# Performance work log

Hardware: AMD Instinct MI355X
Metric: run time of the kernel (lower is better)

Reference implementation:

```python
import jax, jax.numpy as jnp
import numpy as np

# ---- static config (from init_kwargs) ----
XB = (-51.2, 51.2, 0.8); YB = (-51.2, 51.2, 0.8); ZB = (-10.0, 10.0, 20.0); DB = (1.0, 60.0, 1.0)
OGH, OGW = 256, 704          # image_size
DS = 16                      # downsample
C_IN, C_TR = 512, 64         # numC_input, numC_trans
B, N = 2, 6                  # batch, cameras
FH, FW = (OGH + DS - 1) // DS, (OGW + DS - 1) // DS   # 16, 44
DBINS = int(np.arange(DB[0], DB[1], DB[2]).shape[0])  # 59 depth bins
NX = int(round((XB[1] - XB[0]) / XB[2]))              # 128
NY = int(round((YB[1] - YB[0]) / YB[2]))              # 128
NZ = int(round((ZB[1] - ZB[0]) / ZB[2]))              # 1
START = jnp.array([XB[0], YB[0], ZB[0]], jnp.float32)
INTERVAL = jnp.array([XB[2], YB[2], ZB[2]], jnp.float32)

def make_frustum():
    ds = np.arange(DB[0], DB[1], DB[2], dtype=np.float32)            # [D]
    xs = np.linspace(0.0, OGW - 1, FW, dtype=np.float32)             # [FW]
    ys = np.linspace(0.0, OGH - 1, FH, dtype=np.float32)             # [FH]
    x, y, d = np.broadcast_arrays(xs[None, None, :], ys[None, :, None], ds[:, None, None])
    return jnp.asarray(np.stack([x, y, d], -1))                      # [D,FH,FW,3]

FRUSTUM = make_frustum()


def setup_inputs() -> dict:
    key = jax.random.key(0)
    k1, k2, k3 = jax.random.split(key, 3)
    x = jax.random.normal(k1, (B, N, C_IN, FH, FW), jnp.float32)
    # camera->ego rotation: cam z -> ego x, cam x -> -ego y, cam y -> -ego z
    R = jnp.array([[0., 0., 1.], [-1., 0., 0.], [0., -1., 0.]], jnp.float32)
    rots = jnp.broadcast_to(R, (B, N, 3, 3))
    trans = 0.5 * jax.random.normal(k2, (B, N, 3), jnp.float32)
    K = jnp.array([[500., 0., OGW / 2.], [0., 500., OGH / 2.], [0., 0., 1.]], jnp.float32)
    intrins = jnp.broadcast_to(K, (B, N, 3, 3))
    fan = C_IN + DBINS + C_TR
    w_depth = jax.random.normal(k3, (DBINS + C_TR, C_IN), jnp.float32) * np.float32(np.sqrt(2.0 / fan))
    b_depth = jnp.zeros((DBINS + C_TR,), jnp.float32)
    return {"x": x, "rots": rots, "trans": trans, "intrins": intrins,
            "w_depth": w_depth, "b_depth": b_depth}


def reference(x, rots, trans, intrins, w_depth, b_depth):
    # ---- geometry: frustum pixel coords -> ego frame (get_geometry) ----
    pts = jnp.concatenate([FRUSTUM[..., :2] * FRUSTUM[..., 2:3], FRUSTUM[..., 2:3]], -1)  # [D,FH,FW,3]
    combine = rots @ jnp.linalg.inv(intrins)                                              # [B,N,3,3]
    geom = jnp.einsum('bnij,dhwj->bndhwi', combine, pts) + trans[:, :, None, None, None, :]
    # ---- depth-weighted feature volume (get_volume) ----
    xf = x.reshape(B * N, C_IN, FH, FW)
    feat = jnp.einsum('oc,bchw->bohw', w_depth, xf) + b_depth[None, :, None, None]        # 1x1 conv
    depth = jax.nn.softmax(feat[:, :DBINS], axis=1)                                       # [BN,D,H,W]
    ctx = feat[:, DBINS:DBINS + C_TR]                                                     # [BN,C,H,W]
    vol = depth[:, None] * ctx[:, :, None]                                                # [BN,C,D,H,W]
    vol = vol.reshape(B, N, C_TR, DBINS, FH, FW).transpose(0, 1, 3, 4, 5, 2)              # [B,N,D,H,W,C]
    # ---- voxel pooling: sort/cumsum trick == per-voxel segment-sum scatter ----
    g = jnp.trunc((geom - START) / INTERVAL).astype(jnp.int32).reshape(-1, 3)             # trunc == torch .long()
    P = g.shape[0]
    b_ix = jnp.repeat(jnp.arange(B, dtype=jnp.int32), P // B)
    kept = ((g[:, 0] >= 0) & (g[:, 0] < NX) & (g[:, 1] >= 0) & (g[:, 1] < NY)
            & (g[:, 2] >= 0) & (g[:, 2] < NZ))
    total = B * NZ * NX * NY
    flat = ((b_ix * NZ + g[:, 2]) * NX + g[:, 0]) * NY + g[:, 1]                          # bev[b,gz,gx,gy]
    flat = jnp.where(kept, flat, total)                                                   # invalid -> dummy slot
    feats = jnp.where(kept[:, None], vol.reshape(-1, C_TR), 0.0)
    bev = jnp.zeros((total + 1, C_TR), vol.dtype).at[flat].add(feats)[:total]
    bev = bev.reshape(B, NZ, NX, NY, C_TR).transpose(0, 4, 1, 2, 3)                       # [B,C,NZ,NX,NY]
    return bev.reshape(B, C_TR * NZ, NX, NY)
```

## Files before the change

### kernel.cpp

```cpp
#include <hip/hip_runtime.h>
#include <cstddef>
#include <cstdint>
#include <math.h>

#define C_IN   512
#define C_TR   64
#define DBINS  59
#define NO     123
#define NOP    128
#define FH     16
#define FW     44
#define NPIX   704
#define NCAM   6
#define NBATCH 2
#define NBN    12
#define NXG    128
#define NYG    128
#define NCH    4
#define KCH    (C_IN/NCH)

#define WS_CMB     0
#define WS_XS      128
#define WS_YS      176

#define WSP_WT     256
#define WT_SZ      (C_IN*NOP)
#define WSP_PART   (WSP_WT + WT_SZ)
#define PART_SZ    (NCH*NBN*NPIX*NOP)
#define WSP_DEP    (WSP_PART + PART_SZ)
#define DEP_SZ     (NBN*NPIX*C_TR)
#define WSP_CTX    (WSP_DEP + DEP_SZ)
#define WSP_BEV    (WSP_CTX + DEP_SZ)
#define BEV_SZ     (NBATCH*NXG*NYG*C_TR)
#define WS_FAST_TOTALF (WSP_BEV + BEV_SZ)

#define WS_FEAT    256
#define WS_CTX     (WS_FEAT + NBN*NOP*NPIX)
#define WS_BEV     (WS_CTX + NBN*NPIX*C_TR)

__device__ void prep_body(const float* __restrict__ rots,
                          const float* __restrict__ intrins,
                          float* __restrict__ wsf, int t)
{
#pragma clang fp contract(off)
  if (t < NBN) {
    const float* K = intrins + t * 9;
    const float* R = rots + t * 9;
    float A[3][3] = {{K[0],K[1],K[2]},{K[3],K[4],K[5]},{K[6],K[7],K[8]}};
    int piv[3] = {0,1,2};
    for (int k = 0; k < 2; ++k) {
      int p = k; float mx = fabsf(A[k][k]);
      for (int r = k+1; r < 3; ++r) { float v = fabsf(A[r][k]); if (v > mx) { mx = v; p = r; } }
      if (p != k) {
        for (int j = 0; j < 3; ++j) { float tmp = A[k][j]; A[k][j] = A[p][j]; A[p][j] = tmp; }
        int ti = piv[k]; piv[k] = piv[p]; piv[p] = ti;
      }
      float rk = 1.0f / A[k][k];
      for (int r = k+1; r < 3; ++r) {
        float l = A[r][k] * rk;
        A[r][k] = l;
        for (int j = k+1; j < 3; ++j) A[r][j] = A[r][j] - l * A[k][j];
      }
    }
    float r0 = 1.0f / A[0][0], r1 = 1.0f / A[1][1], r2 = 1.0f / A[2][2];
    float inv[3][3];
    for (int j = 0; j < 3; ++j) {
      float b0 = (piv[0]==j) ? 1.0f : 0.0f;
      float b1 = (piv[1]==j) ? 1.0f : 0.0f;
      float b2 = (piv[2]==j) ? 1.0f : 0.0f;
      float y0 = b0;
      float y1 = b1 - A[1][0]*y0;
      float y2 = (b2 - A[2][0]*y0) - A[2][1]*y1;
      float x2 = y2 * r2;
      float x1 = (y1 - A[1][2]*x2) * r1;
      float x0 = ((y0 - A[0][1]*x1) - A[0][2]*x2) * r0;
      inv[0][j] = x0; inv[1][j] = x1; inv[2][j] = x2;
    }
    float* cm = wsf + WS_CMB + t * 9;
    #pragma unroll
    for (int i = 0; i < 3; ++i)
      #pragma unroll
      for (int j = 0; j < 3; ++j)
        cm[i*3+j] = (R[i*3+0]*inv[0][j] + R[i*3+1]*inv[1][j]) + R[i*3+2]*inv[2][j];
  }
  if (t < FW) wsf[WS_XS + t] = (t == FW-1) ? 703.0f : (float)((double)t * (703.0 / 43.0));
  if (t < FH) wsf[WS_YS + t] = (t == FH-1) ? 255.0f : (float)((double)t * 17.0);
}

__global__ __launch_bounds__(256) void zero_prep_kernel(
    float4* __restrict__ bevp, int n4,
    const float* __restrict__ rots, const float* __restrict__ intrins,
    const float* __restrict__ w, float* __restrict__ wT,
    float* __restrict__ wsf)
{
  int i = blockIdx.x * 256 + threadIdx.x;
  const int stride = gridDim.x * 256;
  for (int j = i; j < n4; j += stride) bevp[j] = make_float4(0.f, 0.f, 0.f, 0.f);
  if (wT) {
    for (int j = i; j < C_IN * NOP; j += stride) {
      int k = j >> 7, o = j & 127;
      wT[j] = (o < NO) ? w[(size_t)o * C_IN + k] : 0.0f;
    }
  }
  if (blockIdx.x == 0 && threadIdx.x < 64)
    prep_body(rots, intrins, wsf, threadIdx.x);
}

__global__ __launch_bounds__(256) void gemm_split_kernel(
    const float* __restrict__ x, const float* __restrict__ wT,
    float* __restrict__ partial)
{
  __shared__ float smem[32 * 128];
  float (*Xs)[32] = (float(*)[32])smem;
  const int bn  = blockIdx.y;
  const int ch  = blockIdx.z;
  const int hw0 = blockIdx.x * 32;
  const int t   = threadIdx.x;
  const int tx  = t & 7;
  const int ty  = t >> 3;
  float acc[4][4] = {};
  const float* xb = x + (size_t)bn * C_IN * NPIX;
  const int k0c = ch * KCH;

  for (int ks = 0; ks < KCH; ks += 32) {
    const int k0 = k0c + ks;
    #pragma unroll
    for (int i = 0; i < 4; ++i) {
      int k = (t >> 5) + i * 8;
      Xs[k][t & 31] = xb[(size_t)(k0 + k) * NPIX + hw0 + (t & 31)];
    }
    __syncthreads();
    const float4* wp = (const float4*)(wT + (size_t)k0 * NOP) + ty;
    #pragma unroll 8
    for (int k = 0; k < 32; ++k) {
      float4 xa = *(const float4*)&Xs[k][tx*4];
      float4 wv = wp[k * 32];
      acc[0][0] += wv.x*xa.x; acc[0][1] += wv.x*xa.y; acc[0][2] += wv.x*xa.z; acc[0][3] += wv.x*xa.w;
      acc[1][0] += wv.y*xa.x; acc[1][1] += wv.y*xa.y; acc[1][2] += wv.y*xa.z; acc[1][3] += wv.y*xa.w;
      acc[2][0] += wv.z*xa.x; acc[2][1] += wv.z*xa.y; acc[2][2] += wv.z*xa.z; acc[2][3] += wv.z*xa.w;
      acc[3][0] += wv.w*xa.x; acc[3][1] += wv.w*xa.y; acc[3][2] += wv.w*xa.z; acc[3][3] += wv.w*xa.w;
    }
    __syncthreads();
  }
  float (*PT)[128] = (float(*)[128])smem;
  #pragma unroll
  for (int j = 0; j < 4; ++j) {
    float4 v = make_float4(acc[0][j], acc[1][j], acc[2][j], acc[3][j]);
    *(float4*)&PT[tx*4 + j][ty*4] = v;
  }
  __syncthreads();
  float* dst = partial + ((size_t)(ch*NBN + bn) * NPIX + hw0) * NOP;
  #pragma unroll
  for (int p = 0; p < 4; ++p) {
    int pix = (t >> 5) + p * 8;
    int o4  = (t & 31) * 4;
    *(float4*)&dst[(size_t)pix * NOP + o4] = *(const float4*)&PT[pix][o4];
  }
}

__global__ __launch_bounds__(256) void combine_kernel(
    const float* __restrict__ partial, const float* __restrict__ bias,
    float* __restrict__ depth, float* __restrict__ ctx_t)
{
  const int gid  = (int)((blockIdx.x * blockDim.x + threadIdx.x) >> 6);
  const int lane = threadIdx.x & 63;
  if (gid >= NBN * NPIX) return;
  const int bn  = gid / NPIX;
  const int pix = gid - bn * NPIX;

  float v0 = 0.0f, v1 = 0.0f;
  #pragma unroll
  for (int ch = 0; ch < NCH; ++ch) {
    const float* p = partial + ((size_t)(ch*NBN + bn) * NPIX + pix) * NOP;
    v0 += p[lane];
    v1 += p[lane + 64];
  }
  v0 += bias[lane];
  v1 += (lane + 64 < NO) ? bias[lane + 64] : 0.0f;

  float logit = (lane < DBINS) ? v0 : -__builtin_inff();
  float m = logit;
  #pragma unroll
  for (int off = 32; off; off >>= 1) m = fmaxf(m, __shfl_xor(m, off, 64));
  float e = (lane < DBINS) ? expf(logit - m) : 0.0f;
  float s = e;
  #pragma unroll
  for (int off = 32; off; off >>= 1) s += __shfl_xor(s, off, 64);

  if (lane < DBINS) depth[(size_t)gid * C_TR + lane] = e / s;

  float a  = __shfl(v0, (DBINS + lane) & 63, 64);
  float b2 = __shfl(v1, (DBINS + lane - 64) & 63, 64);
  float ctxv = (lane < 5) ? a : b2;
  ctx_t[(size_t)gid * C_TR + lane] = ctxv;
}

__global__ __launch_bounds__(256) void agg_kernel(
    const float* __restrict__ wsf, const float* __restrict__ trans,
    const float* __restrict__ dep, const float* __restrict__ ctx,
    float* __restrict__ bev, size_t sBN, size_t sD, size_t sP)
{
#pragma clang fp contract(off)
  const int wid = (int)((blockIdx.x * blockDim.x + threadIdx.x) >> 6);
  const int lane = threadIdx.x & 63;
  if (wid >= NBN * FW * DBINS) return;
  const int bn  = wid / (FW * DBINS);
  const int rem = wid - bn * (FW * DBINS);
  const int col = rem / DBINS;
  const int dm1 = rem - col * DBINS;
  const int b   = bn / NCAM;

  const float* cm = wsf + WS_CMB + bn * 9;
  const float* tr = trans + bn * 3;
  const float dd = 1.0f + (float)dm1;
  const float px = wsf[WS_XS + col] * dd;
  const float py0 = wsf[WS_YS + 0] * dd;
  const float e0 = (cm[0]*px + cm[1]*py0) + cm[2]*dd;
  const float e1 = (cm[3]*px + cm[4]*py0) + cm[5]*dd;
  const float g0 = e0 + tr[0];
  const float g1 = e1 + tr[1];
  const int gx = (int)truncf((g0 + 51.2f) / 0.8f);
  const int gy = (int)truncf((g1 + 51.2f) / 0.8f);
  if (gx < 0 || gx >= NXG || gy < 0 || gy >= NYG) return;

  const int r = lane & 15;
  const float pyr = wsf[WS_YS + r] * dd;
  const float e2 = (cm[6]*px + cm[7]*pyr) + cm[8]*dd;
  const float g2 = e2 + tr[2];
  const int gz = (int)truncf((g2 + 10.0f) / 20.0f);
  unsigned long long mask = __ballot(gz == 0) & 0xFFFFull;
  if (mask == 0) return;

  const float dep_r = dep[(size_t)bn * sBN + (size_t)dm1 * sD + (size_t)(r*FW + col) * sP];
  const float* ctxbase = ctx + ((size_t)bn * NPIX + col) * C_TR + lane;

  float acc = 0.0f;
  #pragma unroll
  for (int row = 0; row < FH; ++row) {
    if ((mask >> row) & 1ull) {
      float dv = __shfl(dep_r, row, 64);
      acc += dv * ctxbase[(size_t)(row * FW) * C_TR];
    }
  }
  atomicAdd(&bev[(((size_t)(b*NXG + gx) * NYG + gy) * C_TR) + lane], acc);
}

__global__ __launch_bounds__(256) void transpose_kernel(
    const float* __restrict__ bev, float* __restrict__ out)
{
  __shared__ float tile[NYG][C_TR + 1];
  const int b  = blockIdx.x >> 7;
  const int gx = blockIdx.x & 127;
  const float* src = bev + ((size_t)(b * NXG + gx) * NYG) * C_TR;
  const int t = threadIdx.x;
  #pragma unroll
  for (int i = 0; i < 32; ++i) {
    int idx = t + i * 256;
    tile[idx >> 6][idx & 63] = src[idx];
  }
  __syncthreads();
  const int lane = t & 63;
  const int cw   = t >> 6;
  size_t obase = (size_t)b * (C_TR*NXG*NYG) + (size_t)gx * NYG;
  #pragma unroll
  for (int i = 0; i < 16; ++i) {
    int c = cw + i * 4;
    out[obase + (size_t)c * (NXG*NYG) + lane]      = tile[lane][c];
    out[obase + (size_t)c * (NXG*NYG) + 64 + lane] = tile[64 + lane][c];
  }
}

__global__ __launch_bounds__(256) void gemm_fb_kernel(
    const float* __restrict__ x, const float* __restrict__ w,
    const float* __restrict__ bias, float* __restrict__ feat,
    float* __restrict__ ctx_t)
{
  __shared__ float Xs[64][32];
  __shared__ float Ws[128][66];
  __shared__ float CtxT[32][C_TR];
  const int bn  = blockIdx.y;
  const int hw0 = blockIdx.x * 32;
  const int t   = threadIdx.x;
  const int tx  = t & 7;
  const int ty  = t >> 3;
  float acc[4][4] = {};
  const float* xb = x + (size_t)bn * C_IN * NPIX;

  for (int k0 = 0; k0 < C_IN; k0 += 64) {
    #pragma unroll
    for (int i = 0; i < 8; ++i) {
      int r = (t >> 5) + i * 8;
      Xs[r][t & 31] = xb[(size_t)(k0 + r) * NPIX + hw0 + (t & 31)];
    }
    #pragma unroll
    for (int i = 0; i < 32; ++i) {
      int o = (t >> 6) + i * 4;
      Ws[o][t & 63] = (o < NO) ? w[(size_t)o * C_IN + k0 + (t & 63)] : 0.0f;
    }
    __syncthreads();
    #pragma unroll 8
    for (int k = 0; k < 64; k += 2) {
      float4 xa = *(const float4*)&Xs[k][tx*4];
      float4 xc = *(const float4*)&Xs[k+1][tx*4];
      #pragma unroll
      for (int i = 0; i < 4; ++i) {
        float2 wv = *(const float2*)&Ws[ty*4+i][k];
        acc[i][0] += wv.x*xa.x; acc[i][1] += wv.x*xa.y;
        acc[i][2] += wv.x*xa.z; acc[i][3] += wv.x*xa.w;
        acc[i][0] += wv.y*xc.x; acc[i][1] += wv.y*xc.y;
        acc[i][2] += wv.y*xc.z; acc[i][3] += wv.y*xc.w;
      }
    }
    __syncthreads();
  }
  #pragma unroll
  for (int i = 0; i < 4; ++i) {
    int o = ty*4 + i;
    float bb = (o < NO) ? bias[o] : 0.0f;
    float4 v = make_float4(acc[i][0]+bb, acc[i][1]+bb, acc[i][2]+bb, acc[i][3]+bb);
    *(float4*)&feat[((size_t)bn * NOP + o) * NPIX + hw0 + tx*4] = v;
    if (o >= DBINS && o < NO) {
      int c = o - DBINS;
      CtxT[tx*4+0][c] = v.x; CtxT[tx*4+1][c] = v.y;
      CtxT[tx*4+2][c] = v.z; CtxT[tx*4+3][c] = v.w;
    }
  }
  __syncthreads();
  const float* src = &CtxT[0][0];
  float* dst = ctx_t + ((size_t)bn * NPIX + hw0) * C_TR;
  #pragma unroll
  for (int k = 0; k < 2; ++k) {
    int f = (t + 256*k) * 4;
    *(float4*)&dst[f] = *(const float4*)&src[f];
  }
}

__global__ __launch_bounds__(256) void softmax_fb_kernel(float* __restrict__ feat)
{
  const int gwid = (int)((blockIdx.x * blockDim.x + threadIdx.x) >> 6);
  const int lane = threadIdx.x & 63;
  if (gwid >= NBN * NPIX) return;
  const int bn = gwid / NPIX;
  const int hw = gwid - bn * NPIX;
  float* fb = feat + (size_t)bn * NOP * NPIX + hw;
  float logit = (lane < DBINS) ? fb[(size_t)lane * NPIX] : -__builtin_inff();
  float m = logit;
  #pragma unroll
  for (int off = 32; off; off >>= 1) m = fmaxf(m, __shfl_xor(m, off, 64));
  float e = (lane < DBINS) ? expf(logit - m) : 0.0f;
  float s = e;
  #pragma unroll
  for (int off = 32; off; off >>= 1) s += __shfl_xor(s, off, 64);
  if (lane < DBINS) fb[(size_t)lane * NPIX] = e / s;
}

extern "C" void kernel_launch(void* const* d_in, const int* in_sizes, int n_in,
                              void* d_out, int out_size, void* d_ws, size_t ws_size,
                              hipStream_t stream)
{
  const float* x       = (const float*)d_in[0];
  const float* rots    = (const float*)d_in[1];
  const float* trans   = (const float*)d_in[2];
  const float* intrins = (const float*)d_in[3];
  const float* wd      = (const float*)d_in[4];
  const float* bd      = (const float*)d_in[5];
  float* out = (float*)d_out;
  float* wsf = (float*)d_ws;

  if (ws_size >= (size_t)WS_FAST_TOTALF * sizeof(float)) {
    float* wT    = wsf + WSP_WT;
    float* part  = wsf + WSP_PART;
    float* depth = wsf + WSP_DEP;
    float* ctx_t = wsf + WSP_CTX;
    float* bev   = wsf + WSP_BEV;
    zero_prep_kernel<<<2048, 256, 0, stream>>>(
        (float4*)bev, BEV_SZ/4, rots, intrins, wd, wT, wsf);
    gemm_split_kernel<<<dim3(NPIX/32, NBN, NCH), 256, 0, stream>>>(x, wT, part);
    combine_kernel<<<(NBN*NPIX)/4, 256, 0, stream>>>(part, bd, depth, ctx_t);
    agg_kernel<<<(NBN*FW*DBINS + 3)/4, 256, 0, stream>>>(
        wsf, trans, depth, ctx_t, bev,
        (size_t)NPIX * C_TR, (size_t)1, (size_t)C_TR);
    transpose_kernel<<<NBATCH*NXG, 256, 0, stream>>>(bev, out);
  } else {
    float* feat  = wsf + WS_FEAT;
    float* ctx_t = wsf + WS_CTX;
    float* bev   = wsf + WS_BEV;
    zero_prep_kernel<<<2048, 256, 0, stream>>>(
        (float4*)bev, BEV_SZ/4, rots, intrins, wd, nullptr, wsf);
    gemm_fb_kernel<<<dim3(NPIX/32, NBN), 256, 0, stream>>>(x, wd, bd, feat, ctx_t);
    softmax_fb_kernel<<<(NBN*NPIX)/4, 256, 0, stream>>>(feat);
    agg_kernel<<<(NBN*FW*DBINS + 3)/4, 256, 0, stream>>>(
        wsf, trans, feat, ctx_t, bev,
        (size_t)NOP * NPIX, (size_t)NPIX, (size_t)1);
    transpose_kernel<<<NBATCH*NXG, 256, 0, stream>>>(bev, out);
  }
}
```

Before: 76.65 us.

## Fuse softmax/combine into voxel aggregation using shared-memory depth and context

Replaces the separate combine and aggregation kernels with one kernel per (camera, column). It reduces split-K partials, computes the depth softmax and context into shared memory, then loops over depth bins to scatter into BEV. This removes one launch and the global write/read of intermediate depth and context buffers. In exchange, the aggregation grid is much smaller, with serial depth-bin loops per wave, which may reduce latency hiding.

```diff
diff --git a/kernel.cpp b/kernel.cpp
--- a/kernel.cpp
+++ b/kernel.cpp
@@ -27,10 +27,7 @@
 #define WT_SZ      (C_IN*NOP)
 #define WSP_PART   (WSP_WT + WT_SZ)
 #define PART_SZ    (NCH*NBN*NPIX*NOP)
-#define WSP_DEP    (WSP_PART + PART_SZ)
-#define DEP_SZ     (NBN*NPIX*C_TR)
-#define WSP_CTX    (WSP_DEP + DEP_SZ)
-#define WSP_BEV    (WSP_CTX + DEP_SZ)
+#define WSP_BEV    (WSP_PART + PART_SZ)
 #define BEV_SZ     (NBATCH*NXG*NYG*C_TR)
 #define WS_FAST_TOTALF (WSP_BEV + BEV_SZ)
 
@@ -158,91 +155,84 @@
   }
 }
 
-__global__ __launch_bounds__(256) void combine_kernel(
+__global__ __launch_bounds__(256) void sm_agg_kernel(
+    const float* __restrict__ wsf, const float* __restrict__ trans,
     const float* __restrict__ partial, const float* __restrict__ bias,
-    float* __restrict__ depth, float* __restrict__ ctx_t)
-{
-  const int gid  = (int)((blockIdx.x * blockDim.x + threadIdx.x) >> 6);
+    float* __restrict__ bev)
+{
+#pragma clang fp contract(off)
+  __shared__ float dep_s[FH][60];
+  __shared__ float ctx_s[FH][C_TR];
+  const int blk  = blockIdx.x;
+  const int bn   = blk / FW;
+  const int col  = blk - bn * FW;
+  const int wave = threadIdx.x >> 6;
   const int lane = threadIdx.x & 63;
-  if (gid >= NBN * NPIX) return;
-  const int bn  = gid / NPIX;
-  const int pix = gid - bn * NPIX;
-
-  float v0 = 0.0f, v1 = 0.0f;
-  #pragma unroll
-  for (int ch = 0; ch < NCH; ++ch) {
-    const float* p = partial + ((size_t)(ch*NBN + bn) * NPIX + pix) * NOP;
-    v0 += p[lane];
-    v1 += p[lane + 64];
-  }
-  v0 += bias[lane];
-  v1 += (lane + 64 < NO) ? bias[lane + 64] : 0.0f;
-
-  float logit = (lane < DBINS) ? v0 : -__builtin_inff();
-  float m = logit;
-  #pragma unroll
-  for (int off = 32; off; off >>= 1) m = fmaxf(m, __shfl_xor(m, off, 64));
-  float e = (lane < DBINS) ? expf(logit - m) : 0.0f;
-  float s = e;
-  #pragma unroll
-  for (int off = 32; off; off >>= 1) s += __shfl_xor(s, off, 64);
-
-  if (lane < DBINS) depth[(size_t)gid * C_TR + lane] = e / s;
-
-  float a  = __shfl(v0, (DBINS + lane) & 63, 64);
-  float b2 = __shfl(v1, (DBINS + lane - 64) & 63, 64);
-  float ctxv = (lane < 5) ? a : b2;
-  ctx_t[(size_t)gid * C_TR + lane] = ctxv;
-}
-
-__global__ __launch_bounds__(256) void agg_kernel(
-    const float* __restrict__ wsf, const float* __restrict__ trans,
-    const float* __restrict__ dep, const float* __restrict__ ctx,
-    float* __restrict__ bev, size_t sBN, size_t sD, size_t sP)
-{
-#pragma clang fp contract(off)
-  const int wid = (int)((blockIdx.x * blockDim.x + threadIdx.x) >> 6);
-  const int lane = threadIdx.x & 63;
-  if (wid >= NBN * FW * DBINS) return;
-  const int bn  = wid / (FW * DBINS);
-  const int rem = wid - bn * (FW * DBINS);
-  const int col = rem / DBINS;
-  const int dm1 = rem - col * DBINS;
-  const int b   = bn / NCAM;
+  const int b    = bn / NCAM;
+
+  #pragma unroll
+  for (int rr = 0; rr < 4; ++rr) {
+    const int row = wave * 4 + rr;
+    const int pix = row * FW + col;
+    float v0 = 0.0f, v1 = 0.0f;
+    #pragma unroll
+    for (int ch = 0; ch < NCH; ++ch) {
+      const float* p = partial + ((size_t)(ch*NBN + bn) * NPIX + pix) * NOP;
+      v0 += p[lane];
+      v1 += p[lane + 64];
+    }
+    v0 += bias[lane];
+    v1 += (lane + 64 < NO) ? bias[lane + 64] : 0.0f;
+
+    float logit = (lane < DBINS) ? v0 : -__builtin_inff();
+    float m = logit;
+    #pragma unroll
+    for (int off = 32; off; off >>= 1) m = fmaxf(m, __shfl_xor(m, off, 64));
+    float e = (lane < DBINS) ? expf(logit - m) : 0.0f;
+    float s = e;
+    #pragma unroll
+    for (int off = 32; off; off >>= 1) s += __shfl_xor(s, off, 64);
+    if (lane < DBINS) dep_s[row][lane] = e / s;
+
+    float a  = __shfl(v0, (DBINS + lane) & 63, 64);
+    float b2 = __shfl(v1, (DBINS + lane - 64) & 63, 64);
+    ctx_s[row][lane] = (lane < 5) ? a : b2;
+  }
+  __syncthreads();
 
   const float* cm = wsf + WS_CMB + bn * 9;
   const float* tr = trans + bn * 3;
-  const float dd = 1.0f + (float)dm1;
-  const float px = wsf[WS_XS + col] * dd;
-  const float py0 = wsf[WS_YS + 0] * dd;
-  const float e0 = (cm[0]*px + cm[1]*py0) + cm[2]*dd;
-  const float e1 = (cm[3]*px + cm[4]*py0) + cm[5]*dd;
-  const float g0 = e0 + tr[0];
-  const float g1 = e1 + tr[1];
-  const int gx = (int)truncf((g0 + 51.2f) / 0.8f);
-  const int gy = (int)truncf((g1 + 51.2f) / 0.8f);
-  if (gx < 0 || gx >= NXG || gy < 0 || gy >= NYG) return;
-
   const int r = lane & 15;
-  const float pyr = wsf[WS_YS + r] * dd;
-  const float e2 = (cm[6]*px + cm[7]*pyr) + cm[8]*dd;
-  const float g2 = e2 + tr[2];
-  const int gz = (int)truncf((g2 + 10.0f) / 20.0f);
-  unsigned long long mask = __ballot(gz == 0) & 0xFFFFull;
-  if (mask == 0) return;
-
-  const float dep_r = dep[(size_t)bn * sBN + (size_t)dm1 * sD + (size_t)(r*FW + col) * sP];
-  const float* ctxbase = ctx + ((size_t)bn * NPIX + col) * C_TR + lane;
-
-  float acc = 0.0f;
-  #pragma unroll
-  for (int row = 0; row < FH; ++row) {
-    if ((mask >> row) & 1ull) {
-      float dv = __shfl(dep_r, row, 64);
-      acc += dv * ctxbase[(size_t)(row * FW) * C_TR];
-    }
-  }
-  atomicAdd(&bev[(((size_t)(b*NXG + gx) * NYG + gy) * C_TR) + lane], acc);
+  for (int dm1 = wave; dm1 < DBINS; dm1 += 4) {
+    const float dd = 1.0f + (float)dm1;
+    const float px = wsf[WS_XS + col] * dd;
+    const float py0 = wsf[WS_YS + 0] * dd;
+    const float e0 = (cm[0]*px + cm[1]*py0) + cm[2]*dd;
+    const float e1 = (cm[3]*px + cm[4]*py0) + cm[5]*dd;
+    const float g0 = e0 + tr[0];
+    const float g1 = e1 + tr[1];
+    const int gx = (int)truncf((g0 + 51.2f) / 0.8f);
+    const int gy = (int)truncf((g1 + 51.2f) / 0.8f);
+    if (gx < 0 || gx >= NXG || gy < 0 || gy >= NYG) continue;
+
+    const float pyr = wsf[WS_YS + r] * dd;
+    const float e2 = (cm[6]*px + cm[7]*pyr) + cm[8]*dd;
+    const float g2 = e2 + tr[2];
+    const int gz = (int)truncf((g2 + 10.0f) / 20.0f);
+    unsigned long long mask = __ballot(gz == 0) & 0xFFFFull;
+    if (mask == 0) continue;
+
+    const float dep_r = dep_s[r][dm1];
+    float acc = 0.0f;
+    #pragma unroll
+    for (int row = 0; row < FH; ++row) {
+      if ((mask >> row) & 1ull) {
+        float dv = __shfl(dep_r, row, 64);
+        acc += dv * ctx_s[row][lane];
+      }
+    }
+    atomicAdd(&bev[(((size_t)(b*NXG + gx) * NYG + gy) * C_TR) + lane], acc);
+  }
 }
 
 __global__ __launch_bounds__(256) void transpose_kernel(
@@ -354,6 +344,56 @@
   if (lane < DBINS) fb[(size_t)lane * NPIX] = e / s;
 }
 
+__global__ __launch_bounds__(256) void agg_kernel(
+    const float* __restrict__ wsf, const float* __restrict__ trans,
+    const float* __restrict__ dep, const float* __restrict__ ctx,
+    float* __restrict__ bev, size_t sBN, size_t sD, size_t sP)
+{
+#pragma clang fp contract(off)
+  const int wid = (int)((blockIdx.x * blockDim.x + threadIdx.x) >> 6);
+  const int lane = threadIdx.x & 63;
+  if (wid >= NBN * FW * DBINS) return;
+  const int bn  = wid / (FW * DBINS);
+  const int rem = wid - bn * (FW * DBINS);
+  const int col = rem / DBINS;
+  const int dm1 = rem - col * DBINS;
+  const int b   = bn / NCAM;
+
+  const float* cm = wsf + WS_CMB + bn * 9;
+  const float* tr = trans + bn * 3;
+  const float dd = 1.0f + (float)dm1;
+  const float px = wsf[WS_XS + col] * dd;
+  const float py0 = wsf[WS_YS + 0] * dd;
+  const float e0 = (cm[0]*px + cm[1]*py0) + cm[2]*dd;
+  const float e1 = (cm[3]*px + cm[4]*py0) + cm[5]*dd;
+  const float g0 = e0 + tr[0];
+  const float g1 = e1 + tr[1];
+  const int gx = (int)truncf((g0 + 51.2f) / 0.8f);
+  const int gy = (int)truncf((g1 + 51.2f) / 0.8f);
+  if (gx < 0 || gx >= NXG || gy < 0 || gy >= NYG) return;
+
+  const int r = lane & 15;
+  const float pyr = wsf[WS_YS + r] * dd;
+  const float e2 = (cm[6]*px + cm[7]*pyr) + cm[8]*dd;
+  const float g2 = e2 + tr[2];
+  const int gz = (int)truncf((g2 + 10.0f) / 20.0f);
+  unsigned long long mask = __ballot(gz == 0) & 0xFFFFull;
+  if (mask == 0) return;
+
+  const float dep_r = dep[(size_t)bn * sBN + (size_t)dm1 * sD + (size_t)(r*FW + col) * sP];
+  const float* ctxbase = ctx + ((size_t)bn * NPIX + col) * C_TR + lane;
+
+  float acc = 0.0f;
+  #pragma unroll
+  for (int row = 0; row < FH; ++row) {
+    if ((mask >> row) & 1ull) {
+      float dv = __shfl(dep_r, row, 64);
+      acc += dv * ctxbase[(size_t)(row * FW) * C_TR];
+    }
+  }
+  atomicAdd(&bev[(((size_t)(b*NXG + gx) * NYG + gy) * C_TR) + lane], acc);
+}
+
 extern "C" void kernel_launch(void* const* d_in, const int* in_sizes, int n_in,
                               void* d_out, int out_size, void* d_ws, size_t ws_size,
                               hipStream_t stream)
@@ -370,16 +410,11 @@
   if (ws_size >= (size_t)WS_FAST_TOTALF * sizeof(float)) {
     float* wT    = wsf + WSP_WT;
     float* part  = wsf + WSP_PART;
-    float* depth = wsf + WSP_DEP;
-    float* ctx_t = wsf + WSP_CTX;
     float* bev   = wsf + WSP_BEV;
     zero_prep_kernel<<<2048, 256, 0, stream>>>(
         (float4*)bev, BEV_SZ/4, rots, intrins, wd, wT, wsf);
     gemm_split_kernel<<<dim3(NPIX/32, NBN, NCH), 256, 0, stream>>>(x, wT, part);
-    combine_kernel<<<(NBN*NPIX)/4, 256, 0, stream>>>(part, bd, depth, ctx_t);
-    agg_kernel<<<(NBN*FW*DBINS + 3)/4, 256, 0, stream>>>(
-        wsf, trans, depth, ctx_t, bev,
-        (size_t)NPIX * C_TR, (size_t)1, (size_t)C_TR);
+    sm_agg_kernel<<<NBN*FW, 256, 0, stream>>>(wsf, trans, part, bd, bev);
     transpose_kernel<<<NBATCH*NXG, 256, 0, stream>>>(bev, out);
   } else {
     float* feat  = wsf + WS_FEAT;
```

Measured after the change: 74.22 us. -3.2%, faster.
